# Kernel optimization log

Measured on AMD Instinct MI355X. Metric: run time of the kernel, lower is better.

Reference implementation:

```python
import jax, jax.numpy as jnp
import numpy as np

D_MODEL = 512
N_HEADS = 8
N_KV_HEADS = 2
HEAD_DIM = 64
PITCH_VOCAB = 128


def setup_inputs() -> dict:
    key = jax.random.key(0)
    ks = jax.random.split(key, 6)
    B, T, P = 2, 256, 12
    s = lambda fan_in: 1.0 / np.sqrt(fan_in)
    hidden_states = jax.random.normal(ks[0], (B, T, P, D_MODEL), dtype=jnp.float32)
    Wq = jax.random.normal(ks[1], (D_MODEL, N_HEADS * HEAD_DIM), dtype=jnp.float32) * s(D_MODEL)
    Wk = jax.random.normal(ks[2], (D_MODEL, N_KV_HEADS * HEAD_DIM), dtype=jnp.float32) * s(D_MODEL)
    Wv = jax.random.normal(ks[3], (D_MODEL, N_KV_HEADS * HEAD_DIM), dtype=jnp.float32) * s(D_MODEL)
    Wo = jax.random.normal(ks[4], (N_HEADS * HEAD_DIM, D_MODEL), dtype=jnp.float32) * s(N_HEADS * HEAD_DIM)
    pitch_table = jax.random.normal(ks[5], (PITCH_VOCAB, HEAD_DIM), dtype=jnp.float32)
    return {"hidden_states": hidden_states, "Wq": Wq, "Wk": Wk, "Wv": Wv, "Wo": Wo, "pitch_table": pitch_table}


def reference(hidden_states, Wq, Wk, Wv, Wo, pitch_table):
    B, T, P, C = hidden_states.shape
    H, Hkv, d = N_HEADS, N_KV_HEADS, HEAD_DIM
    rep = H // Hkv

    q = (hidden_states @ Wq).reshape(B, T, P, H, d)
    k = (hidden_states @ Wk).reshape(B, T, P, Hkv, d)
    v = (hidden_states @ Wv).reshape(B, T, P, Hkv, d)

    # GQA repeat_kv: (B,T,P,Hkv,d) -> (B,T,P,H,d)
    k = jnp.repeat(k, rep, axis=3)
    v = jnp.repeat(v, rep, axis=3)

    # additive pitch bias on q and k
    pitch_emb = pitch_table[jnp.arange(P)]  # (P, d)
    bias = pitch_emb[None, None, :, None, :]
    q = q + bias
    k = k + bias

    # flatten (T,P) -> S and move heads forward: (B,H,S,d)
    S = T * P
    q = q.transpose(0, 3, 1, 2, 4).reshape(B, H, S, d)
    k = k.transpose(0, 3, 1, 2, 4).reshape(B, H, S, d)
    v = v.transpose(0, 3, 1, 2, 4).reshape(B, H, S, d)

    scale = 1.0 / jnp.sqrt(jnp.asarray(d, dtype=q.dtype))
    attn = jax.nn.softmax(jnp.einsum('bhqd,bhkd->bhqk', q, k) * scale, axis=-1)
    out = jnp.einsum('bhqk,bhkd->bhqd', attn, v)  # (B,H,S,d)

    out = out.reshape(B, H, T, P, d).transpose(0, 2, 3, 1, 4).reshape(B, T, P, H * d)
    return out @ Wo
```

## Files before the change

kernel.cpp:

```cpp
#include <hip/hip_runtime.h>
#include <hip/hip_fp16.h>

#define B_   2
#define T_   256
#define P_   12
#define C_   512
#define H_   8
#define HKV_ 2
#define D_   64
#define S_   (T_ * P_)
#define M_   (B_ * S_)
#define NQKV 768

typedef _Float16 half8_t __attribute__((ext_vector_type(8)));
typedef _Float16 half4_t __attribute__((ext_vector_type(4)));
typedef _Float16 half2_t __attribute__((ext_vector_type(2)));
typedef float    float4_t __attribute__((ext_vector_type(4)));

#if __has_builtin(__builtin_amdgcn_exp2f)
#define EXP2(x) __builtin_amdgcn_exp2f(x)
#else
#define EXP2(x) __expf((x) * 0.69314718f)
#endif

#define SOFT_SHIFT 20.0f
#define SOFT_CLAMP 35.5f
#define QSCALE (0.125f * 1.44269504f)

__global__ __launch_bounds__(256) void prep_kernel(
    const float* __restrict__ hs,
    const float* __restrict__ Wq, const float* __restrict__ Wk,
    const float* __restrict__ Wv, const float* __restrict__ Wo,
    _Float16* __restrict__ hs16,
    _Float16* __restrict__ wcatT,
    _Float16* __restrict__ woT)
{
    const int blk = blockIdx.x;
    const int tid = threadIdx.x;

    if (blk < 160) {
        __shared__ __attribute__((aligned(16))) _Float16 Ts[64][72];
        int t, K, Ndst;
        const float* src; int srcN, col0; _Float16* dst;
        if (blk < 96) { t = blk; K = 512; Ndst = 768; dst = wcatT;
            int nt = t / 8;
            int kt = t % 8;
            int n0 = nt * 64, k0 = kt * 64;
            if (n0 < 512)      { src = Wq; srcN = 512; col0 = n0; }
            else if (n0 < 640) { src = Wk; srcN = 128; col0 = n0 - 512; }
            else               { src = Wv; srcN = 128; col0 = n0 - 640; }
#pragma unroll
            for (int i = 0; i < 4; ++i) {
                int row = i * 16 + (tid >> 4);
                int cg  = tid & 15;
                float4_t v = *(const float4_t*)(src + (size_t)(k0 + row) * srcN + col0 + cg * 4);
                Ts[cg * 4 + 0][row] = (_Float16)v[0];
                Ts[cg * 4 + 1][row] = (_Float16)v[1];
                Ts[cg * 4 + 2][row] = (_Float16)v[2];
                Ts[cg * 4 + 3][row] = (_Float16)v[3];
            }
            __syncthreads();
#pragma unroll
            for (int i = 0; i < 2; ++i) {
                int seg = i * 256 + tid;
                int row = seg >> 3, s = seg & 7;
                *(half8_t*)(dst + (size_t)(n0 + row) * K + k0 + s * 8) =
                    *(const half8_t*)&Ts[row][s * 8];
            }
        } else { t = blk - 96; K = 512; dst = woT;
            int nt = t / 8, kt = t % 8;
            int n0 = nt * 64, k0 = kt * 64;
#pragma unroll
            for (int i = 0; i < 4; ++i) {
                int row = i * 16 + (tid >> 4);
                int cg  = tid & 15;
                float4_t v = *(const float4_t*)(Wo + (size_t)(k0 + row) * 512 + n0 + cg * 4);
                Ts[cg * 4 + 0][row] = (_Float16)v[0];
                Ts[cg * 4 + 1][row] = (_Float16)v[1];
                Ts[cg * 4 + 2][row] = (_Float16)v[2];
                Ts[cg * 4 + 3][row] = (_Float16)v[3];
            }
            __syncthreads();
#pragma unroll
            for (int i = 0; i < 2; ++i) {
                int seg = i * 256 + tid;
                int row = seg >> 3, s = seg & 7;
                *(half8_t*)(dst + (size_t)(n0 + row) * K + k0 + s * 8) =
                    *(const half8_t*)&Ts[row][s * 8];
            }
        }
    } else {
        int base = (blk - 160) * 4096;
#pragma unroll
        for (int i = 0; i < 16; ++i) {
            int f4 = base + i * 256 + tid;
            float4_t v = *(const float4_t*)(hs + (size_t)f4 * 4);
            half4_t hv;
            hv[0] = (_Float16)v[0]; hv[1] = (_Float16)v[1];
            hv[2] = (_Float16)v[2]; hv[3] = (_Float16)v[3];
            *(half4_t*)(hs16 + (size_t)f4 * 4) = hv;
        }
    }
}

__global__ __launch_bounds__(256) void qkv_kernel(
    const _Float16* __restrict__ A,
    const _Float16* __restrict__ WT,
    const float* __restrict__ pitch,
    _Float16* __restrict__ qb,
    _Float16* __restrict__ kb,
    _Float16* __restrict__ vb)
{
    const int m0   = blockIdx.x * 64;
    const int n0   = blockIdx.y * 64;
    const int tid  = threadIdx.x;
    const int wave = tid >> 6;
    const int lane = tid & 63;
    const int ln   = lane & 15;
    const int quad = lane >> 4;

    __shared__ __attribute__((aligned(16))) _Float16 As[64][72];
    __shared__ __attribute__((aligned(16))) _Float16 Bs[64][72];

    float4_t acc[4];
#pragma unroll
    for (int nt = 0; nt < 4; ++nt) acc[nt] = (float4_t){0.f, 0.f, 0.f, 0.f};

    const int srow = tid >> 3;
    const int ss   = tid & 7;

    half8_t ar[2], br[2];
#pragma unroll
    for (int i = 0; i < 2; ++i) {
        int row = i * 32 + srow;
        ar[i] = *(const half8_t*)&A [(size_t)(m0 + row) * 512 + ss * 8];
        br[i] = *(const half8_t*)&WT[(size_t)(n0 + row) * 512 + ss * 8];
    }

    for (int k0 = 0; k0 < 512; k0 += 64) {
        __syncthreads();
#pragma unroll
        for (int i = 0; i < 2; ++i) {
            int row = i * 32 + srow;
            *(half8_t*)&As[row][ss * 8] = ar[i];
            *(half8_t*)&Bs[row][ss * 8] = br[i];
        }
        __syncthreads();

        if (k0 + 64 < 512) {
#pragma unroll
            for (int i = 0; i < 2; ++i) {
                int row = i * 32 + srow;
                ar[i] = *(const half8_t*)&A [(size_t)(m0 + row) * 512 + k0 + 64 + ss * 8];
                br[i] = *(const half8_t*)&WT[(size_t)(n0 + row) * 512 + k0 + 64 + ss * 8];
            }
        }

#pragma unroll
        for (int ks = 0; ks < 2; ++ks) {
            half8_t afrag = *(const half8_t*)&As[wave * 16 + ln][ks * 32 + quad * 8];
#pragma unroll
            for (int nt = 0; nt < 4; ++nt) {
                half8_t bfrag = *(const half8_t*)&Bs[nt * 16 + ln][ks * 32 + quad * 8];
                acc[nt] = __builtin_amdgcn_mfma_f32_16x16x32_f16(afrag, bfrag, acc[nt], 0, 0, 0);
            }
        }
    }

    const int region = (n0 < 512) ? 0 : (n0 < 640 ? 1 : 2);
#pragma unroll
    for (int nt = 0; nt < 4; ++nt) {
        int n = n0 + nt * 16 + ln;
#pragma unroll
        for (int r = 0; r < 4; ++r) {
            int m = m0 + wave * 16 + quad * 4 + r;
            int b = m / S_;
            int s = m - b * S_;
            int p = s % P_;
            float v = acc[nt][r];
            if (region == 0) {
                int h = n >> 6, dd = n & 63;
                v = (v + pitch[p * 64 + dd]) * QSCALE;
                qb[(((size_t)(b * H_ + h)) * S_ + s) * 64 + dd] = (_Float16)v;
            } else if (region == 1) {
                int nn = n - 512, h = nn >> 6, dd = nn & 63;
                v = v + pitch[p * 64 + dd];
                kb[(((size_t)(b * HKV_ + h)) * S_ + s) * 64 + dd] = (_Float16)v;
            } else {
                int nn = n - 640, h = nn >> 6, dd = nn & 63;
                vb[(((size_t)(b * HKV_ + h)) * 64 + dd) * S_ + s] = (_Float16)v;
            }
        }
    }
}

__global__ __launch_bounds__(256) void attn_kernel(
    const _Float16* __restrict__ qbuf,
    const _Float16* __restrict__ kbuf,
    const _Float16* __restrict__ vtb,
    _Float16* __restrict__ ob)
{
    const int qblk = blockIdx.x;
    const int bh   = blockIdx.y;
    const int b    = bh >> 3;
    const int h    = bh & 7;
    const int hkv  = h >> 2;
    const int tid  = threadIdx.x;
    const int w    = tid >> 6;
    const int lane = tid & 63;
    const int ln   = lane & 15;
    const int quad = lane >> 4;

    const _Float16* Q  = qbuf + ((size_t)(b * H_ + h)) * S_ * 64;
    const _Float16* K  = kbuf + ((size_t)(b * HKV_ + hkv)) * S_ * 64;
    const _Float16* Vt = vtb  + ((size_t)(b * HKV_ + hkv)) * 64 * S_;

    __shared__ __attribute__((aligned(16))) _Float16 Ks[64][80];
    __shared__ __attribute__((aligned(16))) _Float16 VT[64][80];
    __shared__ __attribute__((aligned(16))) _Float16 Ps[4][32][40];

    const int qbase = qblk * 64 + (w & 1) * 32;
    const int kk0   = (w >> 1) * 32;

    half8_t qfrag[2][2];
#pragma unroll
    for (int sub = 0; sub < 2; ++sub)
#pragma unroll
        for (int ks = 0; ks < 2; ++ks)
            qfrag[sub][ks] = *(const half8_t*)&Q[(size_t)(qbase + sub * 16 + ln) * 64 + ks * 32 + quad * 8];

    float4_t o[2][4];
#pragma unroll
    for (int sub = 0; sub < 2; ++sub)
#pragma unroll
        for (int nt = 0; nt < 4; ++nt) o[sub][nt] = (float4_t){0.f, 0.f, 0.f, 0.f};
    float lr[2][4] = {{0.f,0.f,0.f,0.f},{0.f,0.f,0.f,0.f}};

    const int j0 = tid >> 3, s0 = tid & 7;
    const int j1 = j0 + 32;
    const int r0 = ((j0 & 1) << 4) | ((j0 >> 5) << 5) | ((j0 >> 1) & 15);
    const int r1 = ((j1 & 1) << 4) | ((j1 >> 5) << 5) | ((j1 >> 1) & 15);

    half8_t kr0, kr1, vr0, vr1;
    kr0 = *(const half8_t*)&K[(size_t)j0 * 64 + s0 * 8];
    kr1 = *(const half8_t*)&K[(size_t)j1 * 64 + s0 * 8];
    vr0 = *(const half8_t*)&Vt[(size_t)j0 * S_ + s0 * 8];
    vr1 = *(const half8_t*)&Vt[(size_t)j1 * S_ + s0 * 8];

    for (int kt = 0; kt < S_; kt += 64) {
        __syncthreads();
        *(half8_t*)&Ks[r0][s0 * 8] = kr0;
        *(half8_t*)&Ks[r1][s0 * 8] = kr1;
        *(half8_t*)&VT[j0][s0 * 8] = vr0;
        *(half8_t*)&VT[j1][s0 * 8] = vr1;
        __syncthreads();

        if (kt + 64 < S_) {
            kr0 = *(const half8_t*)&K[(size_t)(kt + 64 + j0) * 64 + s0 * 8];
            kr1 = *(const half8_t*)&K[(size_t)(kt + 64 + j1) * 64 + s0 * 8];
            vr0 = *(const half8_t*)&Vt[(size_t)j0 * S_ + kt + 64 + s0 * 8];
            vr1 = *(const half8_t*)&Vt[(size_t)j1 * S_ + kt + 64 + s0 * 8];
        }

        float4_t sf[2][2];
#pragma unroll
        for (int c = 0; c < 2; ++c) {
            sf[c][0] = (float4_t){0.f, 0.f, 0.f, 0.f};
            sf[c][1] = (float4_t){0.f, 0.f, 0.f, 0.f};
#pragma unroll
            for (int ks = 0; ks < 2; ++ks) {
                half8_t kf = *(const half8_t*)&Ks[kk0 + c * 16 + ln][ks * 32 + quad * 8];
                sf[c][0] = __builtin_amdgcn_mfma_f32_16x16x32_f16(qfrag[0][ks], kf, sf[c][0], 0, 0, 0);
                sf[c][1] = __builtin_amdgcn_mfma_f32_16x16x32_f16(qfrag[1][ks], kf, sf[c][1], 0, 0, 0);
            }
        }

#pragma unroll
        for (int sub = 0; sub < 2; ++sub) {
#pragma unroll
            for (int r = 0; r < 4; ++r) {
                float p0 = EXP2(fminf(sf[0][sub][r], SOFT_CLAMP) - SOFT_SHIFT);
                float p1 = EXP2(fminf(sf[1][sub][r], SOFT_CLAMP) - SOFT_SHIFT);
                lr[sub][r] += p0 + p1;
                half2_t w2; w2[0] = (_Float16)p0; w2[1] = (_Float16)p1;
                *(half2_t*)&Ps[w][sub * 16 + quad * 4 + r][2 * ln] = w2;
            }
        }

        half8_t pf0 = *(const half8_t*)&Ps[w][ln][quad * 8];
        half8_t pf1 = *(const half8_t*)&Ps[w][16 + ln][quad * 8];
#pragma unroll
        for (int nt = 0; nt < 4; ++nt) {
            half8_t vf = *(const half8_t*)&VT[nt * 16 + ln][kk0 + quad * 8];
            o[0][nt] = __builtin_amdgcn_mfma_f32_16x16x32_f16(pf0, vf, o[0][nt], 0, 0, 0);
            o[1][nt] = __builtin_amdgcn_mfma_f32_16x16x32_f16(pf1, vf, o[1][nt], 0, 0, 0);
        }
    }

    __syncthreads();
    if (w >= 2) {
        float* od = (w == 2) ? (float*)&Ks[0][0] : (float*)&VT[0][0];
#pragma unroll
        for (int sub = 0; sub < 2; ++sub)
#pragma unroll
            for (int nt = 0; nt < 4; ++nt)
                *(float4_t*)&od[lane * 32 + (sub * 4 + nt) * 4] = o[sub][nt];
        float* ld = (float*)&Ps[0][0][0] + (w - 2) * 512;
#pragma unroll
        for (int sub = 0; sub < 2; ++sub)
#pragma unroll
            for (int r = 0; r < 4; ++r)
                ld[lane * 8 + sub * 4 + r] = lr[sub][r];
    }
    __syncthreads();
    if (w < 2) {
        const float* os = (w == 0) ? (const float*)&Ks[0][0] : (const float*)&VT[0][0];
        const float* ls = (const float*)&Ps[0][0][0] + w * 512;
#pragma unroll
        for (int sub = 0; sub < 2; ++sub) {
#pragma unroll
            for (int r = 0; r < 4; ++r) {
                float l = lr[sub][r] + ls[lane * 8 + sub * 4 + r];
                l += __shfl_xor(l, 1);
                l += __shfl_xor(l, 2);
                l += __shfl_xor(l, 4);
                l += __shfl_xor(l, 8);
                float inv = 1.0f / l;
                int qg = qbase + sub * 16 + quad * 4 + r;
                size_t base = ((size_t)(b * S_ + qg)) * 512 + h * 64;
#pragma unroll
                for (int nt = 0; nt < 4; ++nt) {
                    float vsum = o[sub][nt][r] + os[lane * 32 + (sub * 4 + nt) * 4 + r];
                    ob[base + nt * 16 + ln] = (_Float16)(vsum * inv);
                }
            }
        }
    }
}

__global__ __launch_bounds__(256) void proj_out_kernel(
    const _Float16* __restrict__ A,
    const _Float16* __restrict__ WT,
    float* __restrict__ outp)
{
    const int m0   = blockIdx.x * 64;
    const int n0   = blockIdx.y * 64;
    const int tid  = threadIdx.x;
    const int wave = tid >> 6;
    const int lane = tid & 63;
    const int ln   = lane & 15;
    const int quad = lane >> 4;

    __shared__ __attribute__((aligned(16))) _Float16 As[64][72];
    __shared__ __attribute__((aligned(16))) _Float16 Bs[64][72];

    float4_t acc[4];
#pragma unroll
    for (int nt = 0; nt < 4; ++nt) acc[nt] = (float4_t){0.f, 0.f, 0.f, 0.f};

    const int srow = tid >> 3;
    const int ss   = tid & 7;

    half8_t ar[2], br[2];
#pragma unroll
    for (int i = 0; i < 2; ++i) {
        int row = i * 32 + srow;
        ar[i] = *(const half8_t*)&A [(size_t)(m0 + row) * 512 + ss * 8];
        br[i] = *(const half8_t*)&WT[(size_t)(n0 + row) * 512 + ss * 8];
    }

    for (int k0 = 0; k0 < 512; k0 += 64) {
        __syncthreads();
#pragma unroll
        for (int i = 0; i < 2; ++i) {
            int row = i * 32 + srow;
            *(half8_t*)&As[row][ss * 8] = ar[i];
            *(half8_t*)&Bs[row][ss * 8] = br[i];
        }
        __syncthreads();

        if (k0 + 64 < 512) {
#pragma unroll
            for (int i = 0; i < 2; ++i) {
                int row = i * 32 + srow;
                ar[i] = *(const half8_t*)&A [(size_t)(m0 + row) * 512 + k0 + 64 + ss * 8];
                br[i] = *(const half8_t*)&WT[(size_t)(n0 + row) * 512 + k0 + 64 + ss * 8];
            }
        }

#pragma unroll
        for (int ks = 0; ks < 2; ++ks) {
            half8_t afrag = *(const half8_t*)&As[wave * 16 + ln][ks * 32 + quad * 8];
#pragma unroll
            for (int nt = 0; nt < 4; ++nt) {
                half8_t bfrag = *(const half8_t*)&Bs[nt * 16 + ln][ks * 32 + quad * 8];
                acc[nt] = __builtin_amdgcn_mfma_f32_16x16x32_f16(afrag, bfrag, acc[nt], 0, 0, 0);
            }
        }
    }

#pragma unroll
    for (int nt = 0; nt < 4; ++nt) {
        int n = n0 + nt * 16 + ln;
#pragma unroll
        for (int r = 0; r < 4; ++r) {
            int m = m0 + wave * 16 + quad * 4 + r;
            outp[(size_t)m * 512 + n] = acc[nt][r];
        }
    }
}

extern "C" void kernel_launch(void* const* d_in, const int* in_sizes, int n_in,
                              void* d_out, int out_size, void* d_ws, size_t ws_size,
                              hipStream_t stream) {
    const float* hs    = (const float*)d_in[0];
    const float* Wq    = (const float*)d_in[1];
    const float* Wk    = (const float*)d_in[2];
    const float* Wv    = (const float*)d_in[3];
    const float* Wo    = (const float*)d_in[4];
    const float* pitch = (const float*)d_in[5];
    float* out = (float*)d_out;

    _Float16* hs16  = (_Float16*)d_ws;
    _Float16* o_buf = hs16;
    _Float16* q_buf = hs16 + (size_t)M_ * 512;
    _Float16* k_buf = q_buf + (size_t)B_ * H_ * S_ * 64;
    _Float16* v_buf = k_buf + (size_t)B_ * HKV_ * S_ * 64;
    _Float16* wcatT = v_buf + (size_t)B_ * HKV_ * S_ * 64;
    _Float16* woT   = wcatT + (size_t)NQKV * 512;

    prep_kernel<<<352, 256, 0, stream>>>(hs, Wq, Wk, Wv, Wo, hs16, wcatT, woT);
    qkv_kernel<<<dim3(M_ / 64, NQKV / 64), 256, 0, stream>>>(hs16, wcatT, pitch, q_buf, k_buf, v_buf);
    attn_kernel<<<dim3(S_ / 64, B_ * H_), 256, 0, stream>>>(q_buf, k_buf, v_buf, o_buf);
    proj_out_kernel<<<dim3(M_ / 64, 8), 256, 0, stream>>>(o_buf, woT, out);
}
```

Measured before the change: 165.6 us.

## Split attention over key halves with combine pass and widen GEMM tiles

Attention now splits the key range into two halves along a third grid dimension. Each half writes a normalized partial output and its row sum, and a new combine kernel merges the halves weighted by those sums. The QKV and output-projection GEMMs move to 64x128 tiles with a 2x4 MFMA per wave for more register reuse. The probability pack uses a packed round-toward-zero convert. This adds an extra pass over the output buffer and more workspace in exchange for more parallelism and better GEMM reuse.

```diff
diff --git a/kernel.cpp b/kernel.cpp
--- a/kernel.cpp
+++ b/kernel.cpp
@@ -11,6 +11,8 @@
 #define S_   (T_ * P_)
 #define M_   (B_ * S_)
 #define NQKV 768
+#define KSPLIT 2
+#define KHALF (S_ / KSPLIT)
 
 typedef _Float16 half8_t __attribute__((ext_vector_type(8)));
 typedef _Float16 half4_t __attribute__((ext_vector_type(4)));
@@ -22,6 +24,14 @@
 #else
 #define EXP2(x) __expf((x) * 0.69314718f)
 #endif
+
+static __device__ inline half2_t pack_h2(float a, float b) {
+#if __has_builtin(__builtin_amdgcn_cvt_pkrtz)
+    return __builtin_bit_cast(half2_t, __builtin_amdgcn_cvt_pkrtz(a, b));
+#else
+    half2_t r; r[0] = (_Float16)a; r[1] = (_Float16)b; return r;
+#endif
+}
 
 #define SOFT_SHIFT 20.0f
 #define SOFT_CLAMP 35.5f
@@ -40,54 +50,36 @@
 
     if (blk < 160) {
         __shared__ __attribute__((aligned(16))) _Float16 Ts[64][72];
-        int t, K, Ndst;
-        const float* src; int srcN, col0; _Float16* dst;
-        if (blk < 96) { t = blk; K = 512; Ndst = 768; dst = wcatT;
-            int nt = t / 8;
-            int kt = t % 8;
-            int n0 = nt * 64, k0 = kt * 64;
+        const float* src; int srcN, col0; _Float16* dst; int n0, k0;
+        if (blk < 96) {
+            int nt = blk / 8, kt = blk % 8;
+            n0 = nt * 64; k0 = kt * 64; dst = wcatT;
             if (n0 < 512)      { src = Wq; srcN = 512; col0 = n0; }
             else if (n0 < 640) { src = Wk; srcN = 128; col0 = n0 - 512; }
             else               { src = Wv; srcN = 128; col0 = n0 - 640; }
-#pragma unroll
-            for (int i = 0; i < 4; ++i) {
-                int row = i * 16 + (tid >> 4);
-                int cg  = tid & 15;
-                float4_t v = *(const float4_t*)(src + (size_t)(k0 + row) * srcN + col0 + cg * 4);
-                Ts[cg * 4 + 0][row] = (_Float16)v[0];
-                Ts[cg * 4 + 1][row] = (_Float16)v[1];
-                Ts[cg * 4 + 2][row] = (_Float16)v[2];
-                Ts[cg * 4 + 3][row] = (_Float16)v[3];
-            }
-            __syncthreads();
-#pragma unroll
-            for (int i = 0; i < 2; ++i) {
-                int seg = i * 256 + tid;
-                int row = seg >> 3, s = seg & 7;
-                *(half8_t*)(dst + (size_t)(n0 + row) * K + k0 + s * 8) =
-                    *(const half8_t*)&Ts[row][s * 8];
-            }
-        } else { t = blk - 96; K = 512; dst = woT;
+        } else {
+            int t = blk - 96;
             int nt = t / 8, kt = t % 8;
-            int n0 = nt * 64, k0 = kt * 64;
-#pragma unroll
-            for (int i = 0; i < 4; ++i) {
-                int row = i * 16 + (tid >> 4);
-                int cg  = tid & 15;
-                float4_t v = *(const float4_t*)(Wo + (size_t)(k0 + row) * 512 + n0 + cg * 4);
-                Ts[cg * 4 + 0][row] = (_Float16)v[0];
-                Ts[cg * 4 + 1][row] = (_Float16)v[1];
-                Ts[cg * 4 + 2][row] = (_Float16)v[2];
-                Ts[cg * 4 + 3][row] = (_Float16)v[3];
-            }
-            __syncthreads();
-#pragma unroll
-            for (int i = 0; i < 2; ++i) {
-                int seg = i * 256 + tid;
-                int row = seg >> 3, s = seg & 7;
-                *(half8_t*)(dst + (size_t)(n0 + row) * K + k0 + s * 8) =
-                    *(const half8_t*)&Ts[row][s * 8];
-            }
+            n0 = nt * 64; k0 = kt * 64; dst = woT;
+            src = Wo; srcN = 512; col0 = n0;
+        }
+#pragma unroll
+        for (int i = 0; i < 4; ++i) {
+            int row = i * 16 + (tid >> 4);
+            int cg  = tid & 15;
+            float4_t v = *(const float4_t*)(src + (size_t)(k0 + row) * srcN + col0 + cg * 4);
+            Ts[cg * 4 + 0][row] = (_Float16)v[0];
+            Ts[cg * 4 + 1][row] = (_Float16)v[1];
+            Ts[cg * 4 + 2][row] = (_Float16)v[2];
+            Ts[cg * 4 + 3][row] = (_Float16)v[3];
+        }
+        __syncthreads();
+#pragma unroll
+        for (int i = 0; i < 2; ++i) {
+            int seg = i * 256 + tid;
+            int row = seg >> 3, s = seg & 7;
+            *(half8_t*)(dst + (size_t)(n0 + row) * 512 + k0 + s * 8) =
+                *(const half8_t*)&Ts[row][s * 8];
         }
     } else {
         int base = (blk - 160) * 4096;
@@ -112,83 +104,93 @@
     _Float16* __restrict__ vb)
 {
     const int m0   = blockIdx.x * 64;
-    const int n0   = blockIdx.y * 64;
+    const int n0   = blockIdx.y * 128;
     const int tid  = threadIdx.x;
-    const int wave = tid >> 6;
+    const int wv   = tid >> 6;
     const int lane = tid & 63;
     const int ln   = lane & 15;
     const int quad = lane >> 4;
+    const int wm   = (wv & 1) * 32;
+    const int wn   = (wv >> 1) * 64;
 
     __shared__ __attribute__((aligned(16))) _Float16 As[64][72];
-    __shared__ __attribute__((aligned(16))) _Float16 Bs[64][72];
-
-    float4_t acc[4];
-#pragma unroll
-    for (int nt = 0; nt < 4; ++nt) acc[nt] = (float4_t){0.f, 0.f, 0.f, 0.f};
+    __shared__ __attribute__((aligned(16))) _Float16 Bs[128][72];
+
+    float4_t acc[2][4];
+#pragma unroll
+    for (int ms = 0; ms < 2; ++ms)
+#pragma unroll
+        for (int nt = 0; nt < 4; ++nt) acc[ms][nt] = (float4_t){0.f, 0.f, 0.f, 0.f};
 
     const int srow = tid >> 3;
     const int ss   = tid & 7;
 
-    half8_t ar[2], br[2];
-#pragma unroll
-    for (int i = 0; i < 2; ++i) {
-        int row = i * 32 + srow;
-        ar[i] = *(const half8_t*)&A [(size_t)(m0 + row) * 512 + ss * 8];
-        br[i] = *(const half8_t*)&WT[(size_t)(n0 + row) * 512 + ss * 8];
-    }
+    half8_t ar[2], br[4];
+#pragma unroll
+    for (int i = 0; i < 2; ++i)
+        ar[i] = *(const half8_t*)&A[(size_t)(m0 + i * 32 + srow) * 512 + ss * 8];
+#pragma unroll
+    for (int i = 0; i < 4; ++i)
+        br[i] = *(const half8_t*)&WT[(size_t)(n0 + i * 32 + srow) * 512 + ss * 8];
 
     for (int k0 = 0; k0 < 512; k0 += 64) {
         __syncthreads();
 #pragma unroll
-        for (int i = 0; i < 2; ++i) {
-            int row = i * 32 + srow;
-            *(half8_t*)&As[row][ss * 8] = ar[i];
-            *(half8_t*)&Bs[row][ss * 8] = br[i];
-        }
+        for (int i = 0; i < 2; ++i) *(half8_t*)&As[i * 32 + srow][ss * 8] = ar[i];
+#pragma unroll
+        for (int i = 0; i < 4; ++i) *(half8_t*)&Bs[i * 32 + srow][ss * 8] = br[i];
         __syncthreads();
 
         if (k0 + 64 < 512) {
 #pragma unroll
-            for (int i = 0; i < 2; ++i) {
-                int row = i * 32 + srow;
-                ar[i] = *(const half8_t*)&A [(size_t)(m0 + row) * 512 + k0 + 64 + ss * 8];
-                br[i] = *(const half8_t*)&WT[(size_t)(n0 + row) * 512 + k0 + 64 + ss * 8];
-            }
+            for (int i = 0; i < 2; ++i)
+                ar[i] = *(const half8_t*)&A[(size_t)(m0 + i * 32 + srow) * 512 + k0 + 64 + ss * 8];
+#pragma unroll
+            for (int i = 0; i < 4; ++i)
+                br[i] = *(const half8_t*)&WT[(size_t)(n0 + i * 32 + srow) * 512 + k0 + 64 + ss * 8];
         }
 
 #pragma unroll
         for (int ks = 0; ks < 2; ++ks) {
-            half8_t afrag = *(const half8_t*)&As[wave * 16 + ln][ks * 32 + quad * 8];
+            half8_t af[2];
+#pragma unroll
+            for (int ms = 0; ms < 2; ++ms)
+                af[ms] = *(const half8_t*)&As[wm + ms * 16 + ln][ks * 32 + quad * 8];
 #pragma unroll
             for (int nt = 0; nt < 4; ++nt) {
-                half8_t bfrag = *(const half8_t*)&Bs[nt * 16 + ln][ks * 32 + quad * 8];
-                acc[nt] = __builtin_amdgcn_mfma_f32_16x16x32_f16(afrag, bfrag, acc[nt], 0, 0, 0);
+                half8_t bf = *(const half8_t*)&Bs[wn + nt * 16 + ln][ks * 32 + quad * 8];
+#pragma unroll
+                for (int ms = 0; ms < 2; ++ms)
+                    acc[ms][nt] = __builtin_amdgcn_mfma_f32_16x16x32_f16(af[ms], bf, acc[ms][nt], 0, 0, 0);
             }
         }
     }
 
     const int region = (n0 < 512) ? 0 : (n0 < 640 ? 1 : 2);
 #pragma unroll
-    for (int nt = 0; nt < 4; ++nt) {
-        int n = n0 + nt * 16 + ln;
-#pragma unroll
-        for (int r = 0; r < 4; ++r) {
-            int m = m0 + wave * 16 + quad * 4 + r;
-            int b = m / S_;
-            int s = m - b * S_;
-            int p = s % P_;
-            float v = acc[nt][r];
-            if (region == 0) {
-                int h = n >> 6, dd = n & 63;
-                v = (v + pitch[p * 64 + dd]) * QSCALE;
-                qb[(((size_t)(b * H_ + h)) * S_ + s) * 64 + dd] = (_Float16)v;
-            } else if (region == 1) {
-                int nn = n - 512, h = nn >> 6, dd = nn & 63;
-                v = v + pitch[p * 64 + dd];
-                kb[(((size_t)(b * HKV_ + h)) * S_ + s) * 64 + dd] = (_Float16)v;
-            } else {
-                int nn = n - 640, h = nn >> 6, dd = nn & 63;
-                vb[(((size_t)(b * HKV_ + h)) * 64 + dd) * S_ + s] = (_Float16)v;
+    for (int ms = 0; ms < 2; ++ms) {
+#pragma unroll
+        for (int nt = 0; nt < 4; ++nt) {
+            int n = n0 + wn + nt * 16 + ln;
+#pragma unroll
+            for (int r = 0; r < 4; ++r) {
+                int m = m0 + wm + ms * 16 + quad * 4 + r;
+                int b = m / S_;
+                int s = m - b * S_;
+                int p = s % P_;
+                float v = acc[ms][nt][r];
+                if (region == 0) {
+                    int h = n >> 6, dd = n & 63;
+                    v = (v + pitch[p * 64 + dd]) * QSCALE;
+                    qb[(((size_t)(b * H_ + h)) * S_ + s) * 64 + dd] = (_Float16)v;
+                } else if (region == 1) {
+                    int nn = n - 512, h = nn >> 6, dd = nn & 63;
+                    v = v + pitch[p * 64 + dd];
+                    kb[(((size_t)(b * HKV_ + h)) * S_ + s) * 64 + dd] = (_Float16)v;
+                } else {
+                    int nn = n - 640, h = nn >> 6, dd = nn & 63;
+                    vb[(((size_t)(b * HKV_ + h)) * 64 + dd) * S_ + s] = (_Float16)v;
+                }
             }
         }
     }
@@ -198,11 +200,15 @@
     const _Float16* __restrict__ qbuf,
     const _Float16* __restrict__ kbuf,
     const _Float16* __restrict__ vtb,
-    _Float16* __restrict__ ob)
+    _Float16* __restrict__ opA,
+    _Float16* __restrict__ opB,
+    float* __restrict__ lpA,
+    float* __restrict__ lpB)
 {
     const int qblk = blockIdx.x;
     const int bh   = blockIdx.y;
-    const int b    = bh >> 3;
+    const int kz   = blockIdx.z;
+    const int bb   = bh >> 3;
     const int h    = bh & 7;
     const int hkv  = h >> 2;
     const int tid  = threadIdx.x;
@@ -211,9 +217,12 @@
     const int ln   = lane & 15;
     const int quad = lane >> 4;
 
-    const _Float16* Q  = qbuf + ((size_t)(b * H_ + h)) * S_ * 64;
-    const _Float16* K  = kbuf + ((size_t)(b * HKV_ + hkv)) * S_ * 64;
-    const _Float16* Vt = vtb  + ((size_t)(b * HKV_ + hkv)) * 64 * S_;
+    _Float16* op = kz ? opB : opA;
+    float*    lp = kz ? lpB : lpA;
+
+    const _Float16* Q  = qbuf + ((size_t)(bb * H_ + h)) * S_ * 64;
+    const _Float16* K  = kbuf + ((size_t)(bb * HKV_ + hkv)) * S_ * 64;
+    const _Float16* Vt = vtb  + ((size_t)(bb * HKV_ + hkv)) * 64 * S_;
 
     __shared__ __attribute__((aligned(16))) _Float16 Ks[64][80];
     __shared__ __attribute__((aligned(16))) _Float16 VT[64][80];
@@ -221,6 +230,7 @@
 
     const int qbase = qblk * 64 + (w & 1) * 32;
     const int kk0   = (w >> 1) * 32;
+    const int ktlo  = kz * KHALF;
 
     half8_t qfrag[2][2];
 #pragma unroll
@@ -242,12 +252,12 @@
     const int r1 = ((j1 & 1) << 4) | ((j1 >> 5) << 5) | ((j1 >> 1) & 15);
 
     half8_t kr0, kr1, vr0, vr1;
-    kr0 = *(const half8_t*)&K[(size_t)j0 * 64 + s0 * 8];
-    kr1 = *(const half8_t*)&K[(size_t)j1 * 64 + s0 * 8];
-    vr0 = *(const half8_t*)&Vt[(size_t)j0 * S_ + s0 * 8];
-    vr1 = *(const half8_t*)&Vt[(size_t)j1 * S_ + s0 * 8];
-
-    for (int kt = 0; kt < S_; kt += 64) {
+    kr0 = *(const half8_t*)&K[(size_t)(ktlo + j0) * 64 + s0 * 8];
+    kr1 = *(const half8_t*)&K[(size_t)(ktlo + j1) * 64 + s0 * 8];
+    vr0 = *(const half8_t*)&Vt[(size_t)j0 * S_ + ktlo + s0 * 8];
+    vr1 = *(const half8_t*)&Vt[(size_t)j1 * S_ + ktlo + s0 * 8];
+
+    for (int kt = ktlo; kt < ktlo + KHALF; kt += 64) {
         __syncthreads();
         *(half8_t*)&Ks[r0][s0 * 8] = kr0;
         *(half8_t*)&Ks[r1][s0 * 8] = kr1;
@@ -255,7 +265,7 @@
         *(half8_t*)&VT[j1][s0 * 8] = vr1;
         __syncthreads();
 
-        if (kt + 64 < S_) {
+        if (kt + 64 < ktlo + KHALF) {
             kr0 = *(const half8_t*)&K[(size_t)(kt + 64 + j0) * 64 + s0 * 8];
             kr1 = *(const half8_t*)&K[(size_t)(kt + 64 + j1) * 64 + s0 * 8];
             vr0 = *(const half8_t*)&Vt[(size_t)j0 * S_ + kt + 64 + s0 * 8];
@@ -282,8 +292,7 @@
                 float p0 = EXP2(fminf(sf[0][sub][r], SOFT_CLAMP) - SOFT_SHIFT);
                 float p1 = EXP2(fminf(sf[1][sub][r], SOFT_CLAMP) - SOFT_SHIFT);
                 lr[sub][r] += p0 + p1;
-                half2_t w2; w2[0] = (_Float16)p0; w2[1] = (_Float16)p1;
-                *(half2_t*)&Ps[w][sub * 16 + quad * 4 + r][2 * ln] = w2;
+                *(half2_t*)&Ps[w][sub * 16 + quad * 4 + r][2 * ln] = pack_h2(p0, p1);
             }
         }
 
@@ -327,15 +336,43 @@
                 l += __shfl_xor(l, 8);
                 float inv = 1.0f / l;
                 int qg = qbase + sub * 16 + quad * 4 + r;
-                size_t base = ((size_t)(b * S_ + qg)) * 512 + h * 64;
+                size_t base = ((size_t)(bb * S_ + qg)) * 512 + h * 64;
 #pragma unroll
                 for (int nt = 0; nt < 4; ++nt) {
                     float vsum = o[sub][nt][r] + os[lane * 32 + (sub * 4 + nt) * 4 + r];
-                    ob[base + nt * 16 + ln] = (_Float16)(vsum * inv);
+                    op[base + nt * 16 + ln] = (_Float16)(vsum * inv);
                 }
-            }
-        }
-    }
+                if (ln == 0)
+                    lp[(size_t)(bb * H_ + h) * S_ + qg] = l;
+            }
+        }
+    }
+}
+
+__global__ __launch_bounds__(256) void combine_kernel(
+    _Float16* __restrict__ opA,
+    const _Float16* __restrict__ opB,
+    const float* __restrict__ lpA,
+    const float* __restrict__ lpB)
+{
+    int i = blockIdx.x * 256 + threadIdx.x;
+    int base = i * 8;
+    int bs  = base >> 9;
+    int col = base & 511;
+    int h   = col >> 6;
+    int b   = (bs >= S_) ? 1 : 0;
+    int q   = bs - b * S_;
+    size_t row = (size_t)(b * H_ + h) * S_ + q;
+    float la = lpA[row], lb = lpB[row];
+    float s  = la + lb;
+    float wa = la / s, wb = lb / s;
+    half8_t a8 = *(const half8_t*)(opA + (size_t)base);
+    half8_t b8 = *(const half8_t*)(opB + (size_t)base);
+    half8_t o8;
+#pragma unroll
+    for (int j = 0; j < 8; ++j)
+        o8[j] = (_Float16)((float)a8[j] * wa + (float)b8[j] * wb);
+    *(half8_t*)(opA + (size_t)base) = o8;
 }
 
 __global__ __launch_bounds__(256) void proj_out_kernel(
@@ -344,68 +381,78 @@
     float* __restrict__ outp)
 {
     const int m0   = blockIdx.x * 64;
-    const int n0   = blockIdx.y * 64;
+    const int n0   = blockIdx.y * 128;
     const int tid  = threadIdx.x;
-    const int wave = tid >> 6;
+    const int wv   = tid >> 6;
     const int lane = tid & 63;
     const int ln   = lane & 15;
     const int quad = lane >> 4;
+    const int wm   = (wv & 1) * 32;
+    const int wn   = (wv >> 1) * 64;
 
     __shared__ __attribute__((aligned(16))) _Float16 As[64][72];
-    __shared__ __attribute__((aligned(16))) _Float16 Bs[64][72];
-
-    float4_t acc[4];
-#pragma unroll
-    for (int nt = 0; nt < 4; ++nt) acc[nt] = (float4_t){0.f, 0.f, 0.f, 0.f};
+    __shared__ __attribute__((aligned(16))) _Float16 Bs[128][72];
+
+    float4_t acc[2][4];
+#pragma unroll
+    for (int ms = 0; ms < 2; ++ms)
+#pragma unroll
+        for (int nt = 0; nt < 4; ++nt) acc[ms][nt] = (float4_t){0.f, 0.f, 0.f, 0.f};
 
     const int srow = tid >> 3;
     const int ss   = tid & 7;
 
-    half8_t ar[2], br[2];
-#pragma unroll
-    for (int i = 0; i < 2; ++i) {
-        int row = i * 32 + srow;
-        ar[i] = *(const half8_t*)&A [(size_t)(m0 + row) * 512 + ss * 8];
-        br[i] = *(const half8_t*)&WT[(size_t)(n0 + row) * 512 + ss * 8];
-    }
+    half8_t ar[2], br[4];
+#pragma unroll
+    for (int i = 0; i < 2; ++i)
+        ar[i] = *(const half8_t*)&A[(size_t)(m0 + i * 32 + srow) * 512 + ss * 8];
+#pragma unroll
+    for (int i = 0; i < 4; ++i)
+        br[i] = *(const half8_t*)&WT[(size_t)(n0 + i * 32 + srow) * 512 + ss * 8];
 
     for (int k0 = 0; k0 < 512; k0 += 64) {
         __syncthreads();
 #pragma unroll
-        for (int i = 0; i < 2; ++i) {
-            int row = i * 32 + srow;
-            *(half8_t*)&As[row][ss * 8] = ar[i];
-            *(half8_t*)&Bs[row][ss * 8] = br[i];
-        }
+        for (int i = 0; i < 2; ++i) *(half8_t*)&As[i * 32 + srow][ss * 8] = ar[i];
+#pragma unroll
+        for (int i = 0; i < 4; ++i) *(half8_t*)&Bs[i * 32 + srow][ss * 8] = br[i];
         __syncthreads();
 
         if (k0 + 64 < 512) {
 #pragma unroll
-            for (int i = 0; i < 2; ++i) {
-                int row = i * 32 + srow;
-                ar[i] = *(const half8_t*)&A [(size_t)(m0 + row) * 512 + k0 + 64 + ss * 8];
-                br[i] = *(const half8_t*)&WT[(size_t)(n0 + row) * 512 + k0 + 64 + ss * 8];
-            }
+            for (int i = 0; i < 2; ++i)
+                ar[i] = *(const half8_t*)&A[(size_t)(m0 + i * 32 + srow) * 512 + k0 + 64 + ss * 8];
+#pragma unroll
+            for (int i = 0; i < 4; ++i)
+                br[i] = *(const half8_t*)&WT[(size_t)(n0 + i * 32 + srow) * 512 + k0 + 64 + ss * 8];
         }
 
 #pragma unroll
         for (int ks = 0; ks < 2; ++ks) {
-            half8_t afrag = *(const half8_t*)&As[wave * 16 + ln][ks * 32 + quad * 8];
+            half8_t af[2];
+#pragma unroll
+            for (int ms = 0; ms < 2; ++ms)
+                af[ms] = *(const half8_t*)&As[wm + ms * 16 + ln][ks * 32 + quad * 8];
 #pragma unroll
             for (int nt = 0; nt < 4; ++nt) {
-                half8_t bfrag = *(const half8_t*)&Bs[nt * 16 + ln][ks * 32 + quad * 8];
-                acc[nt] = __builtin_amdgcn_mfma_f32_16x16x32_f16(afrag, bfrag, acc[nt], 0, 0, 0);
-            }
-        }
-    }
-
-#pragma unroll
-    for (int nt = 0; nt < 4; ++nt) {
-        int n = n0 + nt * 16 + ln;
-#pragma unroll
-        for (int r = 0; r < 4; ++r) {
-            int m = m0 + wave * 16 + quad * 4 + r;
-            outp[(size_t)m * 512 + n] = acc[nt][r];
+                half8_t bf = *(const half8_t*)&Bs[wn + nt * 16 + ln][ks * 32 + quad * 8];
+#pragma unroll
+                for (int ms = 0; ms < 2; ++ms)
+                    acc[ms][nt] = __builtin_amdgcn_mfma_f32_16x16x32_f16(af[ms], bf, acc[ms][nt], 0, 0, 0);
+            }
+        }
+    }
+
+#pragma unroll
+    for (int ms = 0; ms < 2; ++ms) {
+#pragma unroll
+        for (int nt = 0; nt < 4; ++nt) {
+            int n = n0 + wn + nt * 16 + ln;
+#pragma unroll
+            for (int r = 0; r < 4; ++r) {
+                int m = m0 + wm + ms * 16 + quad * 4 + r;
+                outp[(size_t)m * 512 + n] = acc[ms][nt][r];
+            }
         }
     }
 }
@@ -422,15 +469,19 @@
     float* out = (float*)d_out;
 
     _Float16* hs16  = (_Float16*)d_ws;
-    _Float16* o_buf = hs16;
+    _Float16* opA   = hs16;
     _Float16* q_buf = hs16 + (size_t)M_ * 512;
     _Float16* k_buf = q_buf + (size_t)B_ * H_ * S_ * 64;
     _Float16* v_buf = k_buf + (size_t)B_ * HKV_ * S_ * 64;
     _Float16* wcatT = v_buf + (size_t)B_ * HKV_ * S_ * 64;
     _Float16* woT   = wcatT + (size_t)NQKV * 512;
+    _Float16* opB   = woT   + (size_t)512 * 512;
+    float*    lpA   = (float*)(opB + (size_t)M_ * 512);
+    float*    lpB   = lpA + (size_t)B_ * H_ * S_;
 
     prep_kernel<<<352, 256, 0, stream>>>(hs, Wq, Wk, Wv, Wo, hs16, wcatT, woT);
-    qkv_kernel<<<dim3(M_ / 64, NQKV / 64), 256, 0, stream>>>(hs16, wcatT, pitch, q_buf, k_buf, v_buf);
-    attn_kernel<<<dim3(S_ / 64, B_ * H_), 256, 0, stream>>>(q_buf, k_buf, v_buf, o_buf);
-    proj_out_kernel<<<dim3(M_ / 64, 8), 256, 0, stream>>>(o_buf, woT, out);
-}
+    qkv_kernel<<<dim3(M_ / 64, NQKV / 128), 256, 0, stream>>>(hs16, wcatT, pitch, q_buf, k_buf, v_buf);
+    attn_kernel<<<dim3(S_ / 64, B_ * H_, KSPLIT), 256, 0, stream>>>(q_buf, k_buf, v_buf, opA, opB, lpA, lpB);
+    combine_kernel<<<(M_ * 512 / 8) / 256, 256, 0, stream>>>(opA, opB, lpA, lpB);
+    proj_out_kernel<<<dim3(M_ / 64, 4), 256, 0, stream>>>(opA, woT, out);
+}
```

New measurement: 181.5 us. 9.6% more time.
